# Kernel tuning notes

Measured on AMD Instinct MI355X. Metric: run time of the kernel, lower is better.

Reference implementation:

```python
import jax, jax.numpy as jnp
import numpy as np

K = 5  # kernel_size per dim (dim=2 -> 25 kernels), B-spline degree 1, open spline


def spline_conv(x, edge_index, pseudo, W, root, bias):
    # x: [N, Cin], pseudo: [E, 2] in [0,1], W: [K*K, Cin, Cout]
    N = x.shape[0]
    src, dst = edge_index[0], edge_index[1]
    # Transform node features with every kernel weight once: [N, K*K, Cout]
    xk = jnp.einsum('ni,kio->nko', x, W)
    # Degree-1 open B-spline basis: v = u*(K-1); frac/1-frac weights over 2 knots per dim
    v = pseudo * (K - 1)
    bot = jnp.floor(v)
    frac = v - bot
    bot = bot.astype(jnp.int32)
    msg = jnp.zeros((src.shape[0], W.shape[2]), dtype=x.dtype)
    for s0 in (0, 1):
        for s1 in (0, 1):
            b0 = frac[:, 0] if s0 else (1.0 - frac[:, 0])
            b1 = frac[:, 1] if s1 else (1.0 - frac[:, 1])
            basis = b0 * b1  # [E]
            idx = (jnp.clip(bot[:, 0] + s0, 0, K - 1)
                   + K * jnp.clip(bot[:, 1] + s1, 0, K - 1))  # [E]
            msg = msg + basis[:, None] * xk[src, idx]  # gather [E, Cout]
    # scatter-max aggregation into target nodes; empty nodes -> 0 (PyG convention)
    agg = jax.ops.segment_max(msg, dst, num_segments=N)
    agg = jnp.where(jnp.isfinite(agg), agg, jnp.zeros_like(agg))
    return agg + x @ root + bias


def setup_inputs() -> dict:
    key = jax.random.key(0)
    ks = jax.random.split(key, 8)
    N, E, C = 50000, 1600000, 64
    Cin = C
    s = 1.0 / np.sqrt(25 * Cin)
    return {
        'x': jax.random.normal(ks[0], (N, C), dtype=jnp.float32),
        'edge_index': jax.random.randint(ks[1], (2, E), 0, N, dtype=jnp.int32),
        'edge_attr': jax.random.uniform(ks[2], (E, 2), dtype=jnp.float32),
        'W1': jax.random.normal(ks[3], (25, C, C), dtype=jnp.float32) * s,
        'root1': jax.random.normal(ks[4], (C, C), dtype=jnp.float32) / np.sqrt(C),
        'bias1': jnp.zeros((C,), dtype=jnp.float32),
        'W2': jax.random.normal(ks[5], (25, C, C), dtype=jnp.float32) * s,
        'root2': jax.random.normal(ks[6], (C, C), dtype=jnp.float32) / np.sqrt(C),
        'bias2': jnp.zeros((C,), dtype=jnp.float32),
    }


def reference(x, edge_index, edge_attr, W1, root1, bias1, W2, root2, bias2):
    h = jax.nn.relu(spline_conv(x, edge_index, edge_attr, W1, root1, bias1))
    out = spline_conv(h, edge_index, edge_attr, W2, root2, bias2)
    return out
```

## Files before the change

### kernel.cpp

```cpp
#include <hip/hip_runtime.h>
#include <hip/hip_bf16.h>
#include <math.h>

#define CHANNELS 64
#define KK 25
#define NBLK 26
#define NCOL (NBLK * CHANNELS)
#define NTILES (NCOL / 16)
#define ROWP 2560
#define CELL_BYTES 8192

typedef __attribute__((ext_vector_type(8))) short bf16x8;
typedef __attribute__((ext_vector_type(4))) float f32x4;
typedef __attribute__((ext_vector_type(2))) float f32x2;
typedef unsigned int u32;

__device__ __forceinline__ u32 f2bfu(float f) {
    u32 u = __float_as_uint(f);
    return (u + 0x7FFFu + ((u >> 16) & 1u)) >> 16;
}
__device__ __forceinline__ short f2bf(float f) { return (short)f2bfu(f); }

__device__ __forceinline__ void async_copy16(const void* g, void* l) {
    __builtin_amdgcn_global_load_lds(
        (const __attribute__((address_space(1))) u32*)g,
        (__attribute__((address_space(3))) u32*)l, 16, 0, 0);
}

template<int N> struct IC { static constexpr int v = N; };
template<int G, int GEND, class F>
__device__ __forceinline__ void unrollg(F f) {
    if constexpr (G < GEND) { f(IC<G>{}); unrollg<G + 1, GEND>(f); }
}

__device__ constexpr int cell_stores(int c) {
    return (c < KK) ? (((c % 5) != 0) ? 4 : 0) : 4;
}


__global__ __launch_bounds__(256) void scan_a(const u32* __restrict__ counts,
                                              u32* __restrict__ bsum, int N) {
    const int t = threadIdx.x;
    const int base = blockIdx.x * 1024 + t * 4;
    uint4 v = make_uint4(0, 0, 0, 0);
    if (base + 3 < N) v = *(const uint4*)(counts + base);
    else {
        if (base < N)     v.x = counts[base];
        if (base + 1 < N) v.y = counts[base + 1];
        if (base + 2 < N) v.z = counts[base + 2];
    }
    u32 s = v.x + v.y + v.z + v.w;
    for (int off = 32; off; off >>= 1) s += __shfl_down(s, off, 64);
    __shared__ u32 red[4];
    if ((t & 63) == 0) red[t >> 6] = s;
    __syncthreads();
    if (t == 0) bsum[blockIdx.x] = red[0] + red[1] + red[2] + red[3];
}

__global__ __launch_bounds__(64) void scan_b(u32* __restrict__ bsum, int nb) {
    const int lane = threadIdx.x;
    u32 run = 0;
    for (int base = 0; base < nb; base += 64) {
        u32 v = (base + lane < nb) ? bsum[base + lane] : 0u;
        const u32 orig = v;
        for (int off = 1; off < 64; off <<= 1) {
            u32 u = __shfl_up(v, off, 64);
            if (lane >= off) v += u;
        }
        if (base + lane < nb) bsum[base + lane] = run + v - orig;
        run += __shfl(v, 63, 64);
    }
}

__global__ __launch_bounds__(256) void scan_c(const u32* __restrict__ counts,
                                              const u32* __restrict__ bsum,
                                              u32* __restrict__ cursor, int N) {
    const int t = threadIdx.x;
    const int base = blockIdx.x * 1024 + t * 4;
    uint4 v = make_uint4(0, 0, 0, 0);
    if (base + 3 < N) v = *(const uint4*)(counts + base);
    else {
        if (base < N)     v.x = counts[base];
        if (base + 1 < N) v.y = counts[base + 1];
        if (base + 2 < N) v.z = counts[base + 2];
    }
    __shared__ u32 ps[256];
    ps[t] = v.x + v.y + v.z + v.w;
    __syncthreads();
    for (int off = 1; off < 256; off <<= 1) {
        u32 u = (t >= off) ? ps[t - off] : 0u;
        __syncthreads();
        ps[t] += u;
        __syncthreads();
    }
    u32 ex = ((t > 0) ? ps[t - 1] : 0u) + bsum[blockIdx.x];
    if (base < N)     cursor[base]     = ex;
    if (base + 1 < N) cursor[base + 1] = ex + v.x;
    if (base + 2 < N) cursor[base + 2] = ex + v.x + v.y;
    if (base + 3 < N) cursor[base + 3] = ex + v.x + v.y + v.z;
    if (base <= N - 1 && N - 1 <= base + 3)
        cursor[N] = ex + v.x + v.y + v.z + v.w;
}

__global__ __launch_bounds__(256) void hist_edges(const int* __restrict__ ei,
                                                  u32* __restrict__ counts,
                                                  u32* __restrict__ rank, int E) {
    const int e0 = blockIdx.x * 1024 + threadIdx.x * 4;
    if (e0 + 3 < E) {
        const int4 d = *(const int4*)(ei + E + e0);
        const u32 r0 = atomicAdd(&counts[d.x], 1u);
        const u32 r1 = atomicAdd(&counts[d.y], 1u);
        const u32 r2 = atomicAdd(&counts[d.z], 1u);
        const u32 r3 = atomicAdd(&counts[d.w], 1u);
        *(uint4*)(rank + e0) = make_uint4(r0, r1, r2, r3);
    } else {
        for (int k = 0; k < 4; ++k)
            if (e0 + k < E)
                rank[e0 + k] = atomicAdd(&counts[ei[E + e0 + k]], 1u);
    }
}


__global__ __launch_bounds__(256) void prep_w(const float* __restrict__ W,
                                              const float* __restrict__ root,
                                              __hip_bfloat16* __restrict__ Wb) {
    int idx = blockIdx.x * 256 + threadIdx.x;
    if (idx >= NTILES * 2 * 64 * 8) return;
    int j = idx & 7;
    int l = (idx >> 3) & 63;
    int q = (idx >> 9) & 1;
    int t = idx >> 10;
    int cell = t >> 2;
    int o    = 4 * (l & 15) + (t & 3);
    int k    = q * 32 + (l >> 4) * 8 + j;
    float src = (cell < KK) ? W[cell * 4096 + k * 64 + o] : root[k * 64 + o];
    ((unsigned short*)Wb)[idx] = (unsigned short)f2bf(src);
}

__global__ __launch_bounds__(256) void gemm_nb(
    const float* __restrict__ X, const __hip_bfloat16* __restrict__ Wb,
    char* __restrict__ XK, float* __restrict__ rootf, int N)
{
    __shared__ __align__(16) char lds[4][2][CELL_BYTES];
    const int lane = threadIdx.x & 63;
    const int wv   = threadIdx.x >> 6;
    const int rb   = blockIdx.x * 64 + wv * 16;
    const int m    = lane & 15;
    const int quad = lane >> 4;
    const int Nm1  = N - 1;

    const int rowc = min(rb + m, Nm1);
    const float* __restrict__ xp = X + (size_t)rowc * CHANNELS + quad * 8;
    float af[16];
    *(float4*)(af)      = *(const float4*)(xp);
    *(float4*)(af + 4)  = *(const float4*)(xp + 4);
    *(float4*)(af + 8)  = *(const float4*)(xp + 32);
    *(float4*)(af + 12) = *(const float4*)(xp + 36);
    bf16x8 A0, A1;
#pragma unroll
    for (int j = 0; j < 8; ++j) { A0[j] = f2bf(af[j]); A1[j] = f2bf(af[8 + j]); }

    const int r0 = rb + quad * 4;
    const char* __restrict__ wbc = (const char*)Wb;
    char* const ldsw = &lds[wv][0][0];

    auto stage = [&](int c, int buf) {
        const char* gsrc = wbc + (size_t)c * CELL_BYTES + lane * 16;
        char* lb = ldsw + buf * CELL_BYTES;
#pragma unroll
        for (int k = 0; k < 8; ++k)
            async_copy16(gsrc + k * 1024, lb + k * 1024);
    };

    u32 prevp[4] = {0u, 0u, 0u, 0u};

    stage(0, 0);
    stage(1, 1);

    unrollg<0, NBLK>([&](auto icc) {
        constexpr int c = decltype(icc)::v;
        constexpr int NC = (c == 0) ? 8
                         : cell_stores(c - 1) + ((c + 1 < NBLK) ? 8 : 0);
        asm volatile("s_waitcnt vmcnt(%0)" :: "i"(NC) : "memory");

        const char* cb = ldsw + (c & 1) * CELL_BYTES + lane * 16;
        f32x4 acc0 = {0.f, 0.f, 0.f, 0.f};
        f32x4 acc1 = {0.f, 0.f, 0.f, 0.f};
        f32x4 acc2 = {0.f, 0.f, 0.f, 0.f};
        f32x4 acc3 = {0.f, 0.f, 0.f, 0.f};
        acc0 = __builtin_amdgcn_mfma_f32_16x16x32_bf16(A0, *(const bf16x8*)(cb),        acc0, 0, 0, 0);
        acc0 = __builtin_amdgcn_mfma_f32_16x16x32_bf16(A1, *(const bf16x8*)(cb + 1024), acc0, 0, 0, 0);
        acc1 = __builtin_amdgcn_mfma_f32_16x16x32_bf16(A0, *(const bf16x8*)(cb + 2048), acc1, 0, 0, 0);
        acc1 = __builtin_amdgcn_mfma_f32_16x16x32_bf16(A1, *(const bf16x8*)(cb + 3072), acc1, 0, 0, 0);
        acc2 = __builtin_amdgcn_mfma_f32_16x16x32_bf16(A0, *(const bf16x8*)(cb + 4096), acc2, 0, 0, 0);
        acc2 = __builtin_amdgcn_mfma_f32_16x16x32_bf16(A1, *(const bf16x8*)(cb + 5120), acc2, 0, 0, 0);
        acc3 = __builtin_amdgcn_mfma_f32_16x16x32_bf16(A0, *(const bf16x8*)(cb + 6144), acc3, 0, 0, 0);
        acc3 = __builtin_amdgcn_mfma_f32_16x16x32_bf16(A1, *(const bf16x8*)(cb + 7168), acc3, 0, 0, 0);

        if constexpr (c < KK) {
            constexpr int d1 = c / 5;
            constexpr int d0 = c % 5;
            u32 pk[4];
#pragma unroll
            for (int i = 0; i < 4; ++i) {
                u32 p = __builtin_amdgcn_cvt_pk_fp8_f32(acc0[i], acc1[i], 0u, false);
                p = __builtin_amdgcn_cvt_pk_fp8_f32(acc2[i], acc3[i], p, true);
                pk[i] = p;
            }
            if constexpr (d0 >= 1) {
#pragma unroll
                for (int i = 0; i < 4; ++i) {
                    const int r = min(r0 + i, Nm1);
                    *(uint2*)(XK + (size_t)r * ROWP
                              + (d1 * 512 + (d0 - 1) * 128) + 8 * m) =
                        make_uint2(prevp[i], pk[i]);
                }
            }
#pragma unroll
            for (int i = 0; i < 4; ++i) prevp[i] = pk[i];
        } else {
#pragma unroll
            for (int i = 0; i < 4; ++i) {
                const int r = min(r0 + i, Nm1);
                *(float4*)(rootf + (size_t)r * CHANNELS + 4 * m) =
                    make_float4(acc0[i], acc1[i], acc2[i], acc3[i]);
            }
        }
        if constexpr (c + 2 < NBLK) {
            asm volatile("s_waitcnt lgkmcnt(0)" ::: "memory");
            stage(c + 2, c & 1);
        }
    });
}

__device__ __forceinline__ uint2 mkrec(int src, float v0f, float v1f) {
    const float v0 = v0f * 4.0f, v1 = v1f * 4.0f;
    const int p0 = max(min((int)floorf(v0), 3), 0);
    const int p1 = max(min((int)floorf(v1), 3), 0);
    const float f0 = v0 - (float)p0;
    const float f1 = v1 - (float)p1;
    const u32 f0q = min((u32)(f0 * 65536.0f), 65535u);
    const u32 f1q = min((u32)(f1 * 65536.0f), 65535u);
    uint2 rec;
    rec.x = (u32)src | ((u32)p0 << 16) | ((u32)p1 << 19);
    rec.y = f0q | (f1q << 16);
    return rec;
}

__global__ __launch_bounds__(256) void edge_scatter(
    const int* __restrict__ ei, const float* __restrict__ ps,
    const u32* __restrict__ rank, const u32* __restrict__ cursor,
    uint2* __restrict__ sorted, int E)
{
    const int e0 = blockIdx.x * 1024 + threadIdx.x * 4;
    if (e0 + 3 < E) {
        const int4 s  = *(const int4*)(ei + e0);
        const int4 d  = *(const int4*)(ei + E + e0);
        const float4 pa = *(const float4*)(ps + 2 * e0);
        const float4 pb = *(const float4*)(ps + 2 * e0 + 4);
        const uint4 rk = *(const uint4*)(rank + e0);
        const u32 c0 = cursor[d.x];
        const u32 c1 = cursor[d.y];
        const u32 c2 = cursor[d.z];
        const u32 c3 = cursor[d.w];
        sorted[c0 + rk.x] = mkrec(s.x, pa.x, pa.y);
        sorted[c1 + rk.y] = mkrec(s.y, pa.z, pa.w);
        sorted[c2 + rk.z] = mkrec(s.z, pb.x, pb.y);
        sorted[c3 + rk.w] = mkrec(s.w, pb.z, pb.w);
    } else {
        for (int k = 0; k < 4; ++k) {
            const int e = e0 + k;
            if (e < E)
                sorted[cursor[ei[E + e]] + rank[e]] =
                    mkrec(ei[e], ps[2 * e], ps[2 * e + 1]);
        }
    }
}

__global__ __launch_bounds__(256) void agg_node_p(
    const uint2* __restrict__ sorted, const u32* __restrict__ cursor,
    const char* __restrict__ XK, const float* __restrict__ rootf,
    const float* __restrict__ bias, float* __restrict__ out, int N, int relu,
    int node_blocks, const float* __restrict__ Wsrc,
    const float* __restrict__ rootsrc, __hip_bfloat16* __restrict__ Wbdst)
{
    if ((int)blockIdx.x >= node_blocks) {
        int idx = ((int)blockIdx.x - node_blocks) * 256 + threadIdx.x;
        if (idx < NTILES * 2 * 64 * 8) {
            int j = idx & 7;
            int l = (idx >> 3) & 63;
            int q = (idx >> 9) & 1;
            int t = idx >> 10;
            int cell = t >> 2;
            int o    = 4 * (l & 15) + (t & 3);
            int k    = q * 32 + (l >> 4) * 8 + j;
            float s = (cell < KK) ? Wsrc[cell * 4096 + k * 64 + o] : rootsrc[k * 64 + o];
            ((unsigned short*)Wbdst)[idx] = (unsigned short)f2bf(s);
        }
        return;
    }
    const int lane = threadIdx.x & 63;
    const int n = blockIdx.x * 4 + (threadIdx.x >> 6);
    if (n >= N) return;
    const int q = lane >> 4, j = lane & 15;
    const int beg = (int)cursor[n];
    const int end = (int)cursor[n + 1];

    float m0 = -INFINITY, m1 = -INFINITY, m2 = -INFINITY, m3 = -INFINITY;
    if (beg < end) {
        const int last = end - 1;
#define GATHP(r, q0, q1)                                                       \
        {                                                                      \
            const char* b_ = XK + (size_t)((r).x & 0xffff) * ROWP + (j << 3);  \
            const int o_ = (((int)((r).x >> 16) & 7)                           \
                            + (((int)((r).x >> 19) & 7) << 2)) << 7;           \
            q0 = *(const uint2*)(b_ + o_);                                     \
            q1 = *(const uint2*)(b_ + o_ + 512);                               \
        }
        uint2 rA = sorted[min(beg + q,      last)];
        uint2 rB = sorted[min(beg + 4 + q,  last)];
        uint2 rC = sorted[min(beg + 8 + q,  last)];
        uint2 ga0, ga1, gb0, gb1, gc0, gc1;
        GATHP(rA, ga0, ga1)
        GATHP(rB, gb0, gb1)
        for (int i = beg; i < end; i += 4) {
            uint2 rD = sorted[min(i + 12 + q, last)];
            GATHP(rC, gc0, gc1)
            const float f0 = (float)(rA.y & 0xffff) * (1.0f / 65536.0f);
            const float f1 = (float)(rA.y >> 16)    * (1.0f / 65536.0f);
            const float w00 = (1.f - f0) * (1.f - f1);
            const float w10 = f0 * (1.f - f1);
            const float w01 = (1.f - f0) * f1;
            const float w11 = f0 * f1;
            f32x2 s01 = __builtin_amdgcn_cvt_pk_f32_fp8(ga0.x, false) * w00
                      + __builtin_amdgcn_cvt_pk_f32_fp8(ga0.y, false) * w10
                      + __builtin_amdgcn_cvt_pk_f32_fp8(ga1.x, false) * w01
                      + __builtin_amdgcn_cvt_pk_f32_fp8(ga1.y, false) * w11;
            f32x2 s23 = __builtin_amdgcn_cvt_pk_f32_fp8(ga0.x, true)  * w00
                      + __builtin_amdgcn_cvt_pk_f32_fp8(ga0.y, true)  * w10
                      + __builtin_amdgcn_cvt_pk_f32_fp8(ga1.x, true)  * w01
                      + __builtin_amdgcn_cvt_pk_f32_fp8(ga1.y, true)  * w11;
            m0 = fmaxf(m0, s01.x); m1 = fmaxf(m1, s01.y);
            m2 = fmaxf(m2, s23.x); m3 = fmaxf(m3, s23.y);
            rA = rB; rB = rC; rC = rD;
            ga0 = gb0; ga1 = gb1;
            gb0 = gc0; gb1 = gc1;
        }
#undef GATHP
    }
    m0 = fmaxf(m0, __shfl_xor(m0, 16, 64)); m0 = fmaxf(m0, __shfl_xor(m0, 32, 64));
    m1 = fmaxf(m1, __shfl_xor(m1, 16, 64)); m1 = fmaxf(m1, __shfl_xor(m1, 32, 64));
    m2 = fmaxf(m2, __shfl_xor(m2, 16, 64)); m2 = fmaxf(m2, __shfl_xor(m2, 32, 64));
    m3 = fmaxf(m3, __shfl_xor(m3, 16, 64)); m3 = fmaxf(m3, __shfl_xor(m3, 32, 64));
    const float a0 = isfinite(m0) ? m0 : 0.f;
    const float a1 = isfinite(m1) ? m1 : 0.f;
    const float a2 = isfinite(m2) ? m2 : 0.f;
    const float a3 = isfinite(m3) ? m3 : 0.f;

    const float4 rv = *(const float4*)(rootf + (size_t)n * CHANNELS + 4 * j);
    const float4 bv = *(const float4*)(bias + 4 * j);
    float r0 = a0 + rv.x + bv.x;
    float r1 = a1 + rv.y + bv.y;
    float r2 = a2 + rv.z + bv.z;
    float r3 = a3 + rv.w + bv.w;
    if (relu) {
        r0 = fmaxf(r0, 0.f); r1 = fmaxf(r1, 0.f);
        r2 = fmaxf(r2, 0.f); r3 = fmaxf(r3, 0.f);
    }
    if (q == 0)
        *(float4*)(out + (size_t)n * CHANNELS + 4 * j) = make_float4(r0, r1, r2, r3);
}

extern "C" void kernel_launch(void* const* d_in, const int* in_sizes, int n_in,
                              void* d_out, int out_size, void* d_ws, size_t ws_size,
                              hipStream_t stream) {
    const float* x     = (const float*)d_in[0];
    const int*   ei    = (const int*)d_in[1];
    const float* ps    = (const float*)d_in[2];
    const float* W1    = (const float*)d_in[3];
    const float* root1 = (const float*)d_in[4];
    const float* bias1 = (const float*)d_in[5];
    const float* W2    = (const float*)d_in[6];
    const float* root2 = (const float*)d_in[7];
    const float* bias2 = (const float*)d_in[8];
    float* out = (float*)d_out;

    const int N = in_sizes[0] / CHANNELS;
    const int E = in_sizes[1] / 2;

    char* ws = (char*)d_ws;
    char* xk = ws;
    size_t off = (size_t)N * ROWP;
    float* h = (float*)(ws + off);
    off += (size_t)N * CHANNELS * sizeof(float);
    float* rootf = (float*)(ws + off);
    off += (size_t)N * CHANNELS * sizeof(float);
    uint2* sorted = (uint2*)(ws + off);
    off += (size_t)E * sizeof(uint2);
    u32* rank = (u32*)(ws + off);
    off += (size_t)E * sizeof(u32);
    u32* counts = (u32*)(ws + off);
    off += (size_t)N * 4;
    __hip_bfloat16* Wb = (__hip_bfloat16*)(ws + off);
    off += (size_t)NTILES * 2 * 64 * 8 * 2;
    u32* cursor = (u32*)(ws + off);
    off += ((size_t)N + 1) * 4;
    u32* bsum = (u32*)(ws + off);

    const int prep_blocks = (NTILES * 2 * 64 * 8 + 255) / 256;
    const int gemm_blocks = (N + 63) / 64;
    const int node_blocks = (N + 3) / 4;
    const int edgeQ_blocks = (E + 1023) / 1024;
    const int scan_blocks = (N + 1023) / 1024;

    hipMemsetAsync(counts, 0, (size_t)N * 4, stream);
    prep_w<<<prep_blocks, 256, 0, stream>>>(W1, root1, Wb);

    hist_edges<<<edgeQ_blocks, 256, 0, stream>>>(ei, counts, rank, E);

    gemm_nb<<<gemm_blocks, 256, 0, stream>>>(x, Wb, xk, rootf, N);

    scan_a<<<scan_blocks, 256, 0, stream>>>(counts, bsum, N);
    scan_b<<<1, 64, 0, stream>>>(bsum, scan_blocks);
    scan_c<<<scan_blocks, 256, 0, stream>>>(counts, bsum, cursor, N);

    edge_scatter<<<edgeQ_blocks, 256, 0, stream>>>(ei, ps, rank, cursor, sorted, E);

    agg_node_p<<<node_blocks + prep_blocks, 256, 0, stream>>>(
        sorted, cursor, xk, rootf, bias1, h, N, 1, node_blocks, W2, root2, Wb);

    gemm_nb<<<gemm_blocks, 256, 0, stream>>>(h, Wb, xk, rootf, N);
    agg_node_p<<<node_blocks, 256, 0, stream>>>(
        sorted, cursor, xk, rootf, bias2, out, N, 0, node_blocks, W2, root2, Wb);
}
```

Baseline: 413.7 us.

## Replace global-atomic counting sort with two-level LDS bucket sort of edges

Edges are grouped by destination using a two-level bucket sort instead of a global counting sort. The old scheme used per-edge global atomic histograms, a three-kernel prefix scan and a random scatter. Now each block histograms its edges into 128-node buckets in LDS, reserves space with one global atomic per bucket, and writes into fixed-capacity bucket regions. A per-bucket kernel then does a local counting sort in LDS and writes the CSR cursor. This cuts global atomics and uncoalesced scatter traffic. The cost is the fixed bucket capacity (5120 edges), which silently clamps overflow. It also caps the number of buckets at 512, so it only works for inputs whose destinations are roughly uniform.

```diff
diff --git a/kernel.cpp b/kernel.cpp
--- a/kernel.cpp
+++ b/kernel.cpp
@@ -10,6 +10,12 @@
 #define ROWP 2560
 #define CELL_BYTES 8192
 
+#define BK_SHIFT 7
+#define BK_W 128
+#define BK_CAP 5120
+#define BK_MAXNB 512
+#define EDGES_PER_BLK 4096
+
 typedef __attribute__((ext_vector_type(8))) short bf16x8;
 typedef __attribute__((ext_vector_type(4))) float f32x4;
 typedef __attribute__((ext_vector_type(2))) float f32x2;
@@ -35,89 +41,6 @@
 
 __device__ constexpr int cell_stores(int c) {
     return (c < KK) ? (((c % 5) != 0) ? 4 : 0) : 4;
-}
-
-
-__global__ __launch_bounds__(256) void scan_a(const u32* __restrict__ counts,
-                                              u32* __restrict__ bsum, int N) {
-    const int t = threadIdx.x;
-    const int base = blockIdx.x * 1024 + t * 4;
-    uint4 v = make_uint4(0, 0, 0, 0);
-    if (base + 3 < N) v = *(const uint4*)(counts + base);
-    else {
-        if (base < N)     v.x = counts[base];
-        if (base + 1 < N) v.y = counts[base + 1];
-        if (base + 2 < N) v.z = counts[base + 2];
-    }
-    u32 s = v.x + v.y + v.z + v.w;
-    for (int off = 32; off; off >>= 1) s += __shfl_down(s, off, 64);
-    __shared__ u32 red[4];
-    if ((t & 63) == 0) red[t >> 6] = s;
-    __syncthreads();
-    if (t == 0) bsum[blockIdx.x] = red[0] + red[1] + red[2] + red[3];
-}
-
-__global__ __launch_bounds__(64) void scan_b(u32* __restrict__ bsum, int nb) {
-    const int lane = threadIdx.x;
-    u32 run = 0;
-    for (int base = 0; base < nb; base += 64) {
-        u32 v = (base + lane < nb) ? bsum[base + lane] : 0u;
-        const u32 orig = v;
-        for (int off = 1; off < 64; off <<= 1) {
-            u32 u = __shfl_up(v, off, 64);
-            if (lane >= off) v += u;
-        }
-        if (base + lane < nb) bsum[base + lane] = run + v - orig;
-        run += __shfl(v, 63, 64);
-    }
-}
-
-__global__ __launch_bounds__(256) void scan_c(const u32* __restrict__ counts,
-                                              const u32* __restrict__ bsum,
-                                              u32* __restrict__ cursor, int N) {
-    const int t = threadIdx.x;
-    const int base = blockIdx.x * 1024 + t * 4;
-    uint4 v = make_uint4(0, 0, 0, 0);
-    if (base + 3 < N) v = *(const uint4*)(counts + base);
-    else {
-        if (base < N)     v.x = counts[base];
-        if (base + 1 < N) v.y = counts[base + 1];
-        if (base + 2 < N) v.z = counts[base + 2];
-    }
-    __shared__ u32 ps[256];
-    ps[t] = v.x + v.y + v.z + v.w;
-    __syncthreads();
-    for (int off = 1; off < 256; off <<= 1) {
-        u32 u = (t >= off) ? ps[t - off] : 0u;
-        __syncthreads();
-        ps[t] += u;
-        __syncthreads();
-    }
-    u32 ex = ((t > 0) ? ps[t - 1] : 0u) + bsum[blockIdx.x];
-    if (base < N)     cursor[base]     = ex;
-    if (base + 1 < N) cursor[base + 1] = ex + v.x;
-    if (base + 2 < N) cursor[base + 2] = ex + v.x + v.y;
-    if (base + 3 < N) cursor[base + 3] = ex + v.x + v.y + v.z;
-    if (base <= N - 1 && N - 1 <= base + 3)
-        cursor[N] = ex + v.x + v.y + v.z + v.w;
-}
-
-__global__ __launch_bounds__(256) void hist_edges(const int* __restrict__ ei,
-                                                  u32* __restrict__ counts,
-                                                  u32* __restrict__ rank, int E) {
-    const int e0 = blockIdx.x * 1024 + threadIdx.x * 4;
-    if (e0 + 3 < E) {
-        const int4 d = *(const int4*)(ei + E + e0);
-        const u32 r0 = atomicAdd(&counts[d.x], 1u);
-        const u32 r1 = atomicAdd(&counts[d.y], 1u);
-        const u32 r2 = atomicAdd(&counts[d.z], 1u);
-        const u32 r3 = atomicAdd(&counts[d.w], 1u);
-        *(uint4*)(rank + e0) = make_uint4(r0, r1, r2, r3);
-    } else {
-        for (int k = 0; k < 4; ++k)
-            if (e0 + k < E)
-                rank[e0 + k] = atomicAdd(&counts[ei[E + e0 + k]], 1u);
-    }
 }
 
 
@@ -137,6 +60,124 @@
     ((unsigned short*)Wb)[idx] = (unsigned short)f2bf(src);
 }
 
+__device__ __forceinline__ uint2 mkrec(int src, float v0f, float v1f) {
+    const float v0 = v0f * 4.0f, v1 = v1f * 4.0f;
+    const int p0 = max(min((int)floorf(v0), 3), 0);
+    const int p1 = max(min((int)floorf(v1), 3), 0);
+    const float f0 = v0 - (float)p0;
+    const float f1 = v1 - (float)p1;
+    const u32 f0q = min((u32)(f0 * 65536.0f), 65535u);
+    const u32 f1q = min((u32)(f1 * 65536.0f), 65535u);
+    uint2 rec;
+    rec.x = (u32)src | ((u32)p0 << 16) | ((u32)p1 << 19);
+    rec.y = f0q | (f1q << 16);
+    return rec;
+}
+
+
+__global__ __launch_bounds__(256) void bucket_scatter(
+    const int* __restrict__ ei, const float* __restrict__ ps,
+    u32* __restrict__ bcur, uint2* __restrict__ bucketed, int E, int NB)
+{
+    __shared__ u32 lhist[BK_MAXNB];
+    __shared__ u32 lbase[BK_MAXNB];
+    const int t = threadIdx.x;
+    const int e0 = blockIdx.x * EDGES_PER_BLK;
+    for (int k = t; k < NB; k += 256) lhist[k] = 0;
+    __syncthreads();
+    u32 pk[16];
+#pragma unroll
+    for (int r = 0; r < 16; ++r) {
+        const int e = e0 + r * 256 + t;
+        u32 v = 0u;
+        if (e < E) {
+            const int bkt = ei[E + e] >> BK_SHIFT;
+            const u32 lr = atomicAdd(&lhist[bkt], 1u);
+            v = ((u32)bkt << 13) | lr;
+        }
+        pk[r] = v;
+    }
+    __syncthreads();
+    for (int k = t; k < NB; k += 256) {
+        const u32 h = lhist[k];
+        lbase[k] = h ? atomicAdd(&bcur[k], h) : 0u;
+    }
+    __syncthreads();
+#pragma unroll
+    for (int r = 0; r < 16; ++r) {
+        const int e = e0 + r * 256 + t;
+        if (e < E) {
+            const u32 v = pk[r];
+            const int bkt = (int)(v >> 13);
+            const u32 lr = v & 0x1FFFu;
+            u32 slot = lbase[bkt] + lr;
+            if (slot >= BK_CAP) slot = BK_CAP - 1;
+            const int src = ei[e];
+            const int dst = ei[E + e];
+            uint2 rec = mkrec(src, ps[2 * e], ps[2 * e + 1]);
+            rec.x |= (u32)(dst & (BK_W - 1)) << 22;
+            bucketed[(size_t)bkt * BK_CAP + slot] = rec;
+        }
+    }
+}
+
+__global__ __launch_bounds__(256) void bucket_bases(
+    const u32* __restrict__ bcur, u32* __restrict__ bbase, int NB)
+{
+    __shared__ u32 tmp[BK_MAXNB];
+    const int t = threadIdx.x;
+    for (int k = t; k < NB; k += 256) tmp[k] = min(bcur[k], (u32)BK_CAP);
+    __syncthreads();
+    if (t == 0) {
+        u32 run = 0;
+        for (int k = 0; k < NB; ++k) { const u32 c = tmp[k]; tmp[k] = run; run += c; }
+    }
+    __syncthreads();
+    for (int k = t; k < NB; k += 256) bbase[k] = tmp[k];
+}
+
+__global__ __launch_bounds__(256) void bucket_sort(
+    const uint2* __restrict__ bucketed, const u32* __restrict__ bcur,
+    const u32* __restrict__ bbase, uint2* __restrict__ sorted,
+    u32* __restrict__ cursor, int N)
+{
+    __shared__ __align__(16) uint2 buf[BK_CAP];
+    __shared__ u32 lhist[BK_W + 1];
+    __shared__ u32 lbase[BK_W + 1];
+    const int b = blockIdx.x;
+    const int t = threadIdx.x;
+    const int cnt = (int)min(bcur[b], (u32)BK_CAP);
+    const u32 gb = bbase[b];
+    const uint2* __restrict__ in = bucketed + (size_t)b * BK_CAP;
+
+    for (int k = t; k <= BK_W; k += 256) lhist[k] = 0;
+    __syncthreads();
+    for (int i = t; i < cnt; i += 256) {
+        const u32 nl = (in[i].x >> 22) & (BK_W - 1);
+        atomicAdd(&lhist[nl], 1u);
+    }
+    __syncthreads();
+    if (t == 0) {
+        u32 run = 0;
+        for (int k = 0; k <= BK_W; ++k) { const u32 c = lhist[k]; lhist[k] = run; run += c; }
+    }
+    __syncthreads();
+    for (int k = t; k <= BK_W; k += 256) lbase[k] = lhist[k];
+    __syncthreads();
+    for (int i = t; i < cnt; i += 256) {
+        const uint2 r = in[i];
+        const u32 nl = (r.x >> 22) & (BK_W - 1);
+        const u32 p = atomicAdd(&lhist[nl], 1u);
+        buf[p] = r;
+    }
+    __syncthreads();
+    for (int i = t; i < cnt; i += 256) sorted[gb + i] = buf[i];
+    for (int k = t; k <= BK_W; k += 256) {
+        const int node = b * BK_W + k;
+        if (node <= N) cursor[node] = gb + lbase[k];
+    }
+}
+
 __global__ __launch_bounds__(256) void gemm_nb(
     const float* __restrict__ X, const __hip_bfloat16* __restrict__ Wb,
     char* __restrict__ XK, float* __restrict__ rootf, int N)
@@ -231,50 +272,6 @@
             stage(c + 2, c & 1);
         }
     });
-}
-
-__device__ __forceinline__ uint2 mkrec(int src, float v0f, float v1f) {
-    const float v0 = v0f * 4.0f, v1 = v1f * 4.0f;
-    const int p0 = max(min((int)floorf(v0), 3), 0);
-    const int p1 = max(min((int)floorf(v1), 3), 0);
-    const float f0 = v0 - (float)p0;
-    const float f1 = v1 - (float)p1;
-    const u32 f0q = min((u32)(f0 * 65536.0f), 65535u);
-    const u32 f1q = min((u32)(f1 * 65536.0f), 65535u);
-    uint2 rec;
-    rec.x = (u32)src | ((u32)p0 << 16) | ((u32)p1 << 19);
-    rec.y = f0q | (f1q << 16);
-    return rec;
-}
-
-__global__ __launch_bounds__(256) void edge_scatter(
-    const int* __restrict__ ei, const float* __restrict__ ps,
-    const u32* __restrict__ rank, const u32* __restrict__ cursor,
-    uint2* __restrict__ sorted, int E)
-{
-    const int e0 = blockIdx.x * 1024 + threadIdx.x * 4;
-    if (e0 + 3 < E) {
-        const int4 s  = *(const int4*)(ei + e0);
-        const int4 d  = *(const int4*)(ei + E + e0);
-        const float4 pa = *(const float4*)(ps + 2 * e0);
-        const float4 pb = *(const float4*)(ps + 2 * e0 + 4);
-        const uint4 rk = *(const uint4*)(rank + e0);
-        const u32 c0 = cursor[d.x];
-        const u32 c1 = cursor[d.y];
-        const u32 c2 = cursor[d.z];
-        const u32 c3 = cursor[d.w];
-        sorted[c0 + rk.x] = mkrec(s.x, pa.x, pa.y);
-        sorted[c1 + rk.y] = mkrec(s.y, pa.z, pa.w);
-        sorted[c2 + rk.z] = mkrec(s.z, pb.x, pb.y);
-        sorted[c3 + rk.w] = mkrec(s.w, pb.z, pb.w);
-    } else {
-        for (int k = 0; k < 4; ++k) {
-            const int e = e0 + k;
-            if (e < E)
-                sorted[cursor[ei[E + e]] + rank[e]] =
-                    mkrec(ei[e], ps[2 * e], ps[2 * e + 1]);
-        }
-    }
 }
 
 __global__ __launch_bounds__(256) void agg_node_p(
@@ -387,6 +384,7 @@
 
     const int N = in_sizes[0] / CHANNELS;
     const int E = in_sizes[1] / 2;
+    const int NB = (N + BK_W - 1) / BK_W;
 
     char* ws = (char*)d_ws;
     char* xk = ws;
@@ -397,34 +395,30 @@
     off += (size_t)N * CHANNELS * sizeof(float);
     uint2* sorted = (uint2*)(ws + off);
     off += (size_t)E * sizeof(uint2);
-    u32* rank = (u32*)(ws + off);
-    off += (size_t)E * sizeof(u32);
-    u32* counts = (u32*)(ws + off);
-    off += (size_t)N * 4;
+    uint2* bucketed = (uint2*)(ws + off);
+    off += (size_t)BK_MAXNB * BK_CAP * sizeof(uint2);
+    u32* bcur = (u32*)(ws + off);
+    off += (size_t)BK_MAXNB * 4;
+    u32* bbase = (u32*)(ws + off);
+    off += (size_t)BK_MAXNB * 4;
     __hip_bfloat16* Wb = (__hip_bfloat16*)(ws + off);
     off += (size_t)NTILES * 2 * 64 * 8 * 2;
     u32* cursor = (u32*)(ws + off);
     off += ((size_t)N + 1) * 4;
-    u32* bsum = (u32*)(ws + off);
 
     const int prep_blocks = (NTILES * 2 * 64 * 8 + 255) / 256;
     const int gemm_blocks = (N + 63) / 64;
     const int node_blocks = (N + 3) / 4;
-    const int edgeQ_blocks = (E + 1023) / 1024;
-    const int scan_blocks = (N + 1023) / 1024;
-
-    hipMemsetAsync(counts, 0, (size_t)N * 4, stream);
+    const int bscat_blocks = (E + EDGES_PER_BLK - 1) / EDGES_PER_BLK;
+
+    hipMemsetAsync(bcur, 0, (size_t)BK_MAXNB * 4, stream);
     prep_w<<<prep_blocks, 256, 0, stream>>>(W1, root1, Wb);
 
-    hist_edges<<<edgeQ_blocks, 256, 0, stream>>>(ei, counts, rank, E);
+    bucket_scatter<<<bscat_blocks, 256, 0, stream>>>(ei, ps, bcur, bucketed, E, NB);
+    bucket_bases<<<1, 256, 0, stream>>>(bcur, bbase, NB);
+    bucket_sort<<<NB, 256, 0, stream>>>(bucketed, bcur, bbase, sorted, cursor, N);
 
     gemm_nb<<<gemm_blocks, 256, 0, stream>>>(x, Wb, xk, rootf, N);
-
-    scan_a<<<scan_blocks, 256, 0, stream>>>(counts, bsum, N);
-    scan_b<<<1, 64, 0, stream>>>(bsum, scan_blocks);
-    scan_c<<<scan_blocks, 256, 0, stream>>>(counts, bsum, cursor, N);
-
-    edge_scatter<<<edgeQ_blocks, 256, 0, stream>>>(ei, ps, rank, cursor, sorted, E);
 
     agg_node_p<<<node_blocks + prep_blocks, 256, 0, stream>>>(
         sorted, cursor, xk, rootf, bias1, h, N, 1, node_blocks, W2, root2, Wb);
```

Result: faster. 366.3 us (-11.5%).
